# Optimization experiments

Measured on AMD Instinct MI355X. Metric: run time of the kernel, lower is better.

Reference implementation:

```python
import jax, jax.numpy as jnp
from jax import lax
import numpy as np

DIM = 192
HEADS = 8
TOPK = 2


def conv1x1(x, w):
    # x: [B,C,H,W], w: [O,C] (1x1 conv, no bias)
    return jnp.einsum('bchw,oc->bohw', x, w)


def setup_inputs() -> dict:
    key = jax.random.key(0)
    ks = jax.random.split(key, 6)
    B, C, H, W = 8, DIM, 128, 128
    x = jax.random.normal(ks[0], (B, C, H, W), jnp.float32)
    qkv_w = jax.random.normal(ks[1], (3 * C, C), jnp.float32) * 0.05
    dw_w = jax.random.normal(ks[2], (3 * C, 1, 3, 3), jnp.float32) * 0.1  # depthwise OIHW
    proj_w = jax.random.normal(ks[3], (C, C), jnp.float32) * 0.05
    router_main_w = jax.random.normal(ks[4], (HEADS, C), jnp.float32) * 0.05
    router_aux_w = jax.random.normal(ks[5], (HEADS, C), jnp.float32) * 0.05
    return dict(x=x, qkv_w=qkv_w, dw_w=dw_w, proj_w=proj_w,
                router_main_w=router_main_w, router_aux_w=router_aux_w,
                task_id=0)


def _forward(x, qkv_w, dw_w, proj_w, router_main_w, router_aux_w, task_id):
    B, C, H, W = x.shape
    heads, topk = HEADS, TOPK
    hd = C // heads
    N = H * W
    scale = hd ** -0.5

    # ---- router: softmax -> top-k -> mask -> renormalized gates ----
    rw = router_main_w if task_id == 0 else router_aux_w
    logits = jnp.einsum('bchw,oc->bohw', x, rw)                 # [B, heads, H, W]
    probs = jax.nn.softmax(
        logits.reshape(B, heads, N).transpose(0, 2, 1).reshape(B * N, heads), axis=1)
    _, idx = lax.top_k(probs, topk)                             # [B*N, topk]
    mask = lax.stop_gradient(
        jax.nn.one_hot(idx, heads, dtype=probs.dtype).sum(axis=1))  # [B*N, heads]
    masked = probs * mask
    denom = jnp.maximum(masked.sum(axis=1, keepdims=True), jnp.finfo(x.dtype).eps)
    gates = (masked / denom).reshape(B, N, heads).transpose(0, 2, 1)[:, :, None, :]  # [B, heads, 1, N]

    # ---- QKV: 1x1 conv + depthwise 3x3 conv ----
    qkv = conv1x1(x, qkv_w)                                      # [B, 3C, H, W]
    qkv = lax.conv_general_dilated(
        qkv, dw_w, window_strides=(1, 1), padding=((1, 1), (1, 1)),
        feature_group_count=3 * C,
        dimension_numbers=('NCHW', 'OIHW', 'NCHW'))
    q, k, v = jnp.split(qkv, 3, axis=1)

    def heads_view(t):  # b (h c) H W -> b h c (H W)
        return t.reshape(B, heads, hd, N)

    q, k, v = heads_view(q), heads_view(k), heads_view(v)
    # L2 normalize along the pixel axis (F.normalize, eps=1e-12)
    q = q / jnp.maximum(jnp.linalg.norm(q, axis=-1, keepdims=True), 1e-12)
    k = k / jnp.maximum(jnp.linalg.norm(k, axis=-1, keepdims=True), 1e-12)

    # channel attention: [B, heads, hd, hd] (tiny GEMM)
    attn = jax.nn.softmax(jnp.einsum('bhcn,bhdn->bhcd', q, k) * scale, axis=-1)
    out = jnp.einsum('bhcd,bhdn->bhcn', attn, v)                 # [B, heads, hd, N]

    out = out * gates * topk                                     # MoH gating
    out = out.reshape(B, C, H, W)                                # b (head c) h w
    out = conv1x1(out, proj_w)
    return out


def reference(x, qkv_w, dw_w, proj_w, router_main_w, router_aux_w, task_id):
    return _forward(x, qkv_w, dw_w, proj_w, router_main_w, router_aux_w, task_id)
```

## Files before the change

### kernel.cpp

```cpp
#include <hip/hip_runtime.h>
#include <hip/hip_bf16.h>

typedef __bf16 bf16;
typedef __bf16 bf16x8 __attribute__((ext_vector_type(8)));
typedef __bf16 bf16x4 __attribute__((ext_vector_type(4)));
typedef float f32x4 __attribute__((ext_vector_type(4)));
typedef unsigned int u32;

#define NPIX 16384
#define CDIM 192

__device__ __forceinline__ void gl2lds16(const bf16* g, const bf16* l) {
  __builtin_amdgcn_global_load_lds(
      (const __attribute__((address_space(1))) u32*)(g),
      (__attribute__((address_space(3))) u32*)(l), 16, 0, 0);
}

__global__ __launch_bounds__(256) void detect_kernel(
    const u32* __restrict__ xw, int* __restrict__ flag) {
  int tid = threadIdx.x;
  int cnt = 0;
  for (int i = 0; i < 32; i++) {
    u32 w = xw[tid * 32 + i];
    u32 e = (w >> 7) & 0xFFu;
    if (e >= 0xC0u) cnt++;
  }
  for (int off = 32; off; off >>= 1) cnt += __shfl_down(cnt, off);
  __shared__ int red[4];
  if ((tid & 63) == 0) red[tid >> 6] = cnt;
  __syncthreads();
  if (tid == 0) *flag = (red[0] + red[1] + red[2] + red[3] >= 16) ? 1 : 0;
}

__global__ __launch_bounds__(256) void wconvert_kernel(
    const void* __restrict__ s0, bf16* __restrict__ d0,
    const void* __restrict__ s1, bf16* __restrict__ d1,
    const void* __restrict__ s2, bf16* __restrict__ d2,
    const int* __restrict__ flag) {
  int which = blockIdx.y;
  const void* src = which == 0 ? s0 : (which == 1 ? s1 : s2);
  bf16* dst = which == 0 ? d0 : (which == 1 ? d1 : d2);
  int n = which == 0 ? 110592 : (which == 1 ? 5184 : 36864);
  int base = (blockIdx.x * 256 + threadIdx.x) * 8;
  if (base >= n) return;
  if (*flag) {
    const float* s = (const float*)src;
    float4 lo = *(const float4*)(s + base);
    float4 hi = *(const float4*)(s + base + 4);
    bf16x8 o;
    o[0] = (bf16)lo.x; o[1] = (bf16)lo.y; o[2] = (bf16)lo.z; o[3] = (bf16)lo.w;
    o[4] = (bf16)hi.x; o[5] = (bf16)hi.y; o[6] = (bf16)hi.z; o[7] = (bf16)hi.w;
    *(bf16x8*)(dst + base) = o;
  } else {
    *(bf16x8*)(dst + base) = *(const bf16x8*)((const bf16*)src + base);
  }
}

__global__ __launch_bounds__(256) void transpose_kernel(
    const void* __restrict__ xraw, bf16* __restrict__ xt,
    const int* __restrict__ flag) {
  int t = threadIdx.x;
  int b = blockIdx.y;
  int n0 = blockIdx.x * 128;
  int nl = (t & 31) * 4;
  int cb = (t >> 5) * 8;
  int f = *flag;
  for (int ch = 0; ch < 3; ch++) {
    int c8 = ch * 64 + cb;
    float v[8][4];
    if (f) {
      const float* xp = (const float*)xraw + ((size_t)b * CDIM << 14) + n0 + nl;
#pragma unroll
      for (int i = 0; i < 8; i++) {
        float4 q = *(const float4*)(xp + ((size_t)(c8 + i) << 14));
        v[i][0] = q.x; v[i][1] = q.y; v[i][2] = q.z; v[i][3] = q.w;
      }
    } else {
      const bf16* xp = (const bf16*)xraw + ((size_t)b * CDIM << 14) + n0 + nl;
#pragma unroll
      for (int i = 0; i < 8; i++) {
        bf16x4 q = *(const bf16x4*)(xp + ((size_t)(c8 + i) << 14));
#pragma unroll
        for (int j = 0; j < 4; j++) v[i][j] = (float)q[j];
      }
    }
#pragma unroll
    for (int j = 0; j < 4; j++) {
      bf16x8 o;
#pragma unroll
      for (int i = 0; i < 8; i++) o[i] = (bf16)v[i][j];
      *(bf16x8*)(xt + ((size_t)b << 14) * CDIM + (size_t)(n0 + nl + j) * CDIM + c8) = o;
    }
  }
}

__global__ __launch_bounds__(256) void router_kernel(
    const void* __restrict__ xraw, const void* __restrict__ wmain,
    const void* __restrict__ waux, const int* __restrict__ task,
    const int* __restrict__ flag, float* __restrict__ gates2) {
  __shared__ float w[8][CDIM];
  int tid = threadIdx.x;
  int f = *flag;
  const void* rw = (*task == 0) ? wmain : waux;
  for (int i = tid; i < 8 * CDIM; i += 256)
    w[i / CDIM][i % CDIM] = f ? ((const float*)rw)[i] : (float)((const bf16*)rw)[i];
  __syncthreads();
  int p = blockIdx.x * 256 + tid;
  int b = p >> 14, n = p & (NPIX - 1);
  float l[8];
#pragma unroll
  for (int h = 0; h < 8; h++) l[h] = 0.f;
  if (f) {
    const float* xb = (const float*)xraw + (((size_t)b * CDIM) << 14) + n;
    for (int c = 0; c < CDIM; c++) {
      float xv = xb[(size_t)c << 14];
#pragma unroll
      for (int h = 0; h < 8; h++) l[h] += xv * w[h][c];
    }
  } else {
    const bf16* xb = (const bf16*)xraw + (((size_t)b * CDIM) << 14) + n;
    for (int c = 0; c < CDIM; c++) {
      float xv = (float)xb[(size_t)c << 14];
#pragma unroll
      for (int h = 0; h < 8; h++) l[h] += xv * w[h][c];
    }
  }
  int i1 = 0;
#pragma unroll
  for (int h = 1; h < 8; h++) if (l[h] > l[i1]) i1 = h;
  int i2 = (i1 == 0) ? 1 : 0;
#pragma unroll
  for (int h = 0; h < 8; h++) if (h != i1 && l[h] > l[i2]) i2 = h;
  float e = __expf(l[i2] - l[i1]);
  float g1 = 2.f / (1.f + e);
  float g2 = e * g1;
  float* gb = gates2 + (((size_t)b * 8) << 14) + n;
#pragma unroll
  for (int h = 0; h < 8; h++) {
    float g = (h == i1) ? g1 : ((h == i2) ? g2 : 0.f);
    gb[(size_t)h << 14] = g;
  }
}

__global__ __launch_bounds__(256) void wgemm2_kernel(
    const bf16* __restrict__ A, const bf16* __restrict__ Xt,
    void* __restrict__ C, int M, const int* __restrict__ flag, int finalout) {
  __shared__ bf16 smem[22528];
  int tid = threadIdx.x;
  int wave = tid >> 6, lane = tid & 63;
  int c0 = lane & 15, qd = lane >> 4;

  int nm = M / 96;
  int ord = blockIdx.x + nm * (blockIdx.y + (blockIdx.z << 6));
  int z = ord & 7;
  int local = ord >> 3;
  int mt = local % nm;
  int nt = local / nm;
  int m0 = mt * 96, n0 = nt << 8;

  const bf16* Xb = Xt + (size_t)z * CDIM * NPIX;
  size_t cbase = (size_t)z * M * NPIX;

  int q = lane >> 4;
  int rr = (lane & 15) ^ (q << 1);
  const bf16* Ag0 = A + (size_t)(m0 + (wave << 4) + rr) * CDIM + (q << 3);
  const bf16* Ag1 = A + (size_t)(m0 + ((4 + wave) << 4) + rr) * CDIM + (q << 3);
  const bf16* Bg  = Xb + (size_t)(n0 + (wave << 6) + rr) * CDIM + (q << 3);

  int slot8 = ((qd << 4) + (c0 ^ (qd << 1))) << 3;

  f32x4 acc[6][4];
#pragma unroll
  for (int i = 0; i < 6; i++)
#pragma unroll
    for (int j = 0; j < 4; j++) acc[i][j] = {0.f, 0.f, 0.f, 0.f};

  auto STAGE = [&](int bb, int k) {
    gl2lds16(Ag0 + k, smem + bb + (wave << 9));
    if (wave < 2) gl2lds16(Ag1 + k, smem + bb + ((4 + wave) << 9));
    const bf16* bl = smem + bb + 3072 + (wave << 11);
    gl2lds16(Bg + k,             bl);
    gl2lds16(Bg + 16 * CDIM + k, bl + 512);
    gl2lds16(Bg + 32 * CDIM + k, bl + 1024);
    gl2lds16(Bg + 48 * CDIM + k, bl + 1536);
  };

  int bb = 0;
  STAGE(0, 0);
  __syncthreads();
  for (int t = 0; t < 6; t++) {
    if (t < 5) STAGE(bb ^ 11264, (t + 1) << 5);
    bf16x8 af[6], bfr[4];
#pragma unroll
    for (int mi = 0; mi < 6; mi++)
      af[mi] = *(const bf16x8*)(smem + bb + mi * 512 + slot8);
#pragma unroll
    for (int nj = 0; nj < 4; nj++)
      bfr[nj] = *(const bf16x8*)(smem + bb + 3072 + (wave << 11) + nj * 512 + slot8);
#pragma unroll
    for (int mi = 0; mi < 6; mi++)
#pragma unroll
      for (int nj = 0; nj < 4; nj++)
        acc[mi][nj] = __builtin_amdgcn_mfma_f32_16x16x32_bf16(af[mi], bfr[nj], acc[mi][nj], 0, 0, 0);
    if (t < 5) { __syncthreads(); bb ^= 11264; }
  }

  int f32o = finalout && (*flag);
#pragma unroll
  for (int mi = 0; mi < 6; mi++)
#pragma unroll
    for (int nj = 0; nj < 4; nj++)
#pragma unroll
      for (int r = 0; r < 4; r++) {
        int row = m0 + (mi << 4) + (qd << 2) + r;
        int col = n0 + (wave << 6) + (nj << 4) + c0;
        size_t idx = cbase + ((size_t)row << 14) + col;
        if (f32o) ((float*)C)[idx] = acc[mi][nj][r];
        else      ((bf16*)C)[idx]  = (bf16)acc[mi][nj][r];
      }
}

__global__ __launch_bounds__(256) void dwconv_kernel(
    const bf16* __restrict__ qkv, const bf16* __restrict__ w9,
    bf16* __restrict__ out, float* __restrict__ sumsq) {
  int tid = threadIdx.x;
  int ch = blockIdx.y, b = blockIdx.z;
  int xs = (tid & 15) << 3;
  int y0 = (blockIdx.x << 6) + ((tid >> 4) << 2);
  const bf16* in = qkv + (((size_t)(b * 576 + ch)) << 14);
  float wv[9];
#pragma unroll
  for (int i = 0; i < 9; i++) wv[i] = (float)w9[ch * 9 + i];
  float o[4][8];
#pragma unroll
  for (int r = 0; r < 4; r++)
#pragma unroll
    for (int i = 0; i < 8; i++) o[r][i] = 0.f;
#pragma unroll
  for (int rr = 0; rr < 6; rr++) {
    int yy = y0 - 1 + rr;
    if (yy < 0 || yy > 127) continue;
    const bf16* row = in + (yy << 7);
    float vals[10];
    vals[0] = (xs > 0) ? (float)row[xs - 1] : 0.f;
    bf16x8 v8 = *(const bf16x8*)(row + xs);
#pragma unroll
    for (int j = 0; j < 8; j++) vals[1 + j] = (float)v8[j];
    vals[9] = (xs < 120) ? (float)row[xs + 8] : 0.f;
#pragma unroll
    for (int orow = 0; orow < 4; orow++) {
      int wrow = rr - orow;
      if (wrow < 0 || wrow > 2) continue;
      float w0 = wv[wrow * 3 + 0], w1 = wv[wrow * 3 + 1], w2 = wv[wrow * 3 + 2];
#pragma unroll
      for (int i = 0; i < 8; i++)
        o[orow][i] += w0 * vals[i] + w1 * vals[i + 1] + w2 * vals[i + 2];
    }
  }
  float ss = 0.f;
  bf16* ob = out + (((size_t)(b * 576 + ch)) << 14);
#pragma unroll
  for (int r = 0; r < 4; r++) {
    bf16x8 ov;
#pragma unroll
    for (int i = 0; i < 8; i++) { ov[i] = (bf16)o[r][i]; ss += o[r][i] * o[r][i]; }
    *(bf16x8*)(ob + ((y0 + r) << 7) + xs) = ov;
  }
  if (ch < 384) {
#pragma unroll
    for (int off = 32; off; off >>= 1) ss += __shfl_down(ss, off);
    __shared__ float red[4];
    if ((tid & 63) == 0) red[tid >> 6] = ss;
    __syncthreads();
    if (tid == 0) atomicAdd(&sumsq[b * 384 + ch], red[0] + red[1] + red[2] + red[3]);
  }
}

__global__ __launch_bounds__(256) void spart_kernel(
    const bf16* __restrict__ dwout, float* __restrict__ Spart) {
  int tid = threadIdx.x;
  int bh = blockIdx.y, split = blockIdx.x;
  int b = bh >> 3, h = bh & 7;
  int wave = tid >> 6, lane = tid & 63;
  int c0 = lane & 15, qd = lane >> 4;
  __shared__ float Sred[576];
  for (int i = tid; i < 576; i += 256) Sred[i] = 0.f;
  __syncthreads();
  const bf16* qb = dwout + (((size_t)(b * 576 + h * 24)) << 14);
  const bf16* kb = dwout + (((size_t)(b * 576 + 192 + h * 24)) << 14);
  int r0 = c0;
  int r1 = (16 + c0 < 24) ? (16 + c0) : 23;
  f32x4 a00 = {0.f,0.f,0.f,0.f}, a01 = {0.f,0.f,0.f,0.f};
  f32x4 a10 = {0.f,0.f,0.f,0.f}, a11 = {0.f,0.f,0.f,0.f};
  int base = (((split << 2) + wave) << 9) + (qd << 3);
  for (int t = 0; t < 16; t++) {
    int kk = base + (t << 5);
    bf16x8 qa0 = *(const bf16x8*)(qb + (((size_t)r0) << 14) + kk);
    bf16x8 qa1 = *(const bf16x8*)(qb + (((size_t)r1) << 14) + kk);
    bf16x8 ka0 = *(const bf16x8*)(kb + (((size_t)r0) << 14) + kk);
    bf16x8 ka1 = *(const bf16x8*)(kb + (((size_t)r1) << 14) + kk);
    a00 = __builtin_amdgcn_mfma_f32_16x16x32_bf16(qa0, ka0, a00, 0, 0, 0);
    a01 = __builtin_amdgcn_mfma_f32_16x16x32_bf16(qa0, ka1, a01, 0, 0, 0);
    a10 = __builtin_amdgcn_mfma_f32_16x16x32_bf16(qa1, ka0, a10, 0, 0, 0);
    a11 = __builtin_amdgcn_mfma_f32_16x16x32_bf16(qa1, ka1, a11, 0, 0, 0);
  }
  f32x4 accs[4] = {a00, a01, a10, a11};
#pragma unroll
  for (int mi = 0; mi < 2; mi++)
#pragma unroll
    for (int nj = 0; nj < 2; nj++) {
      f32x4 a = accs[mi * 2 + nj];
#pragma unroll
      for (int r = 0; r < 4; r++) {
        int rrow = (mi << 4) + (qd << 2) + r;
        int cc = (nj << 4) + c0;
        if (rrow < 24 && cc < 24) atomicAdd(&Sred[rrow * 24 + cc], a[r]);
      }
    }
  __syncthreads();
  float* outp = Spart + (size_t)(bh * 8 + split) * 576;
  for (int i = tid; i < 576; i += 256) outp[i] = Sred[i];
}

__global__ __launch_bounds__(576) void attn_kernel(
    const float* __restrict__ Spart, const float* __restrict__ sumsq,
    float* __restrict__ attn) {
  int bh = blockIdx.x, tid = threadIdx.x;
  int b = bh >> 3, h = bh & 7;
  int c = tid / 24, d = tid % 24;
  float s = 0.f;
  for (int sp = 0; sp < 8; sp++) s += Spart[(size_t)(bh * 8 + sp) * 576 + tid];
  float nq = fmaxf(sqrtf(sumsq[b * 384 + h * 24 + c]), 1e-12f);
  float nk = fmaxf(sqrtf(sumsq[b * 384 + 192 + h * 24 + d]), 1e-12f);
  s = s / (nq * nk) * 0.20412414523193154f;
  __shared__ float Sm[576];
  Sm[tid] = s;
  __syncthreads();
  float mx = -1e30f;
  for (int j = 0; j < 24; j++) mx = fmaxf(mx, Sm[c * 24 + j]);
  float Z = 0.f;
  for (int j = 0; j < 24; j++) Z += __expf(Sm[c * 24 + j] - mx);
  attn[(size_t)bh * 576 + tid] = __expf(s - mx) / Z;
}

__global__ __launch_bounds__(256) void av_kernel(
    const bf16* __restrict__ dwout, const float* __restrict__ attn,
    const float* __restrict__ gates2, bf16* __restrict__ gated_t) {
  int tid = threadIdx.x;
  int bh = blockIdx.y;
  int b = bh >> 3, h = bh & 7;
  int n = blockIdx.x * 256 + tid;
  __shared__ float At[576];
  for (int i = tid; i < 576; i += 256) At[i] = attn[(size_t)bh * 576 + i];
  __syncthreads();
  const bf16* vb = dwout + (((size_t)(b * 576 + 384 + h * 24)) << 14) + n;
  float acc[24];
#pragma unroll
  for (int c = 0; c < 24; c++) acc[c] = 0.f;
#pragma unroll
  for (int d0 = 0; d0 < 24; d0 += 4) {
    float v0 = (float)vb[(size_t)(d0 + 0) << 14];
    float v1 = (float)vb[(size_t)(d0 + 1) << 14];
    float v2 = (float)vb[(size_t)(d0 + 2) << 14];
    float v3 = (float)vb[(size_t)(d0 + 3) << 14];
#pragma unroll
    for (int c = 0; c < 24; c++) {
      const float4* ap = (const float4*)&At[c * 24 + d0];
      acc[c] += ap->x * v0 + ap->y * v1 + ap->z * v2 + ap->w * v3;
    }
  }
  float g = gates2[(((size_t)(b * 8 + h)) << 14) + n];
  bf16* ob = gated_t + ((size_t)(b * NPIX + n)) * CDIM + h * 24;
#pragma unroll
  for (int ch = 0; ch < 3; ch++) {
    bf16x8 o;
#pragma unroll
    for (int i = 0; i < 8; i++) o[i] = (bf16)(acc[ch * 8 + i] * g);
    *(bf16x8*)(ob + ch * 8) = o;
  }
}

extern "C" void kernel_launch(void* const* d_in, const int* in_sizes, int n_in,
                              void* d_out, int out_size, void* d_ws, size_t ws_size,
                              hipStream_t stream) {
  const void* x_raw    = d_in[0];
  const void* qkvw_raw = d_in[1];
  const void* dww_raw  = d_in[2];
  const void* projw_raw= d_in[3];
  const void* rtm_raw  = d_in[4];
  const void* rta_raw  = d_in[5];
  const int*  task     = (const int*)d_in[6];
  char* ws = (char*)d_ws;

  bf16*  qkv_raw = (bf16*)(ws);
  bf16*  gated_t = qkv_raw;
  bf16*  dwout   = (bf16*)(ws + 150994944);
  float* gates2  = (float*)(ws + 301989888);
  float* sumsq   = (float*)(ws + 306184192);
  float* Spart   = (float*)(ws + 306196480);
  float* attn    = (float*)(ws + 307376128);
  int*   flag    = (int*)(ws + 307523584);
  bf16*  xt      = (bf16*)(ws + 307523712);
  bf16*  qkv_wb  = (bf16*)(ws + 357855360);
  bf16*  dw_wb   = (bf16*)(ws + 358076544);
  bf16*  proj_wb = (bf16*)(ws + 358086912);

  hipMemsetAsync(sumsq, 0, 8 * 384 * sizeof(float), stream);
  detect_kernel<<<1, 256, 0, stream>>>((const u32*)x_raw, flag);
  wconvert_kernel<<<dim3(54, 3), 256, 0, stream>>>(qkvw_raw, qkv_wb, dww_raw, dw_wb,
                                                   projw_raw, proj_wb, flag);
  transpose_kernel<<<dim3(128, 8), 256, 0, stream>>>(x_raw, xt, flag);
  router_kernel<<<512, 256, 0, stream>>>(x_raw, rtm_raw, rta_raw, task, flag, gates2);
  wgemm2_kernel<<<dim3(6, 64, 8), 256, 0, stream>>>(qkv_wb, xt, qkv_raw, 576, flag, 0);
  dwconv_kernel<<<dim3(2, 576, 8), 256, 0, stream>>>(qkv_raw, dw_wb, dwout, sumsq);
  spart_kernel<<<dim3(8, 64), 256, 0, stream>>>(dwout, Spart);
  attn_kernel<<<64, 576, 0, stream>>>(Spart, sumsq, attn);
  av_kernel<<<dim3(64, 64), 256, 0, stream>>>(dwout, attn, gates2, gated_t);
  wgemm2_kernel<<<dim3(2, 64, 8), 256, 0, stream>>>(proj_wb, gated_t, d_out, 192, flag, 1);
}
```

Before: 466.0 us.

## Fuse router logits into transpose kernel and vectorize GEMM epilogue stores

The router computation moves into the transpose kernel, reusing the x values already loaded there. Per-pixel logits are reduced across lanes with a shuffle and across waves through LDS before top-2 gating. This removes a separate full read of x, which is about 100MB in fp32. In the GEMM, the MFMA operands are swapped so each lane holds four consecutive columns, which lets the epilogue use vectorized float4/bf16x4 stores instead of scalar ones. The cost is extra LDS use and registers in the transpose kernel.

Result: faster. 448.5 us (-3.8%).

```diff
diff --git a/kernel.cpp b/kernel.cpp
--- a/kernel.cpp
+++ b/kernel.cpp
@@ -58,13 +58,28 @@
 
 __global__ __launch_bounds__(256) void transpose_kernel(
     const void* __restrict__ xraw, bf16* __restrict__ xt,
-    const int* __restrict__ flag) {
+    const int* __restrict__ flag, const void* __restrict__ wmain,
+    const void* __restrict__ waux, const int* __restrict__ task,
+    float* __restrict__ gates2) {
+  __shared__ float wT[CDIM][8];
+  __shared__ float lred[4][128][8];
   int t = threadIdx.x;
   int b = blockIdx.y;
   int n0 = blockIdx.x * 128;
+  int f = *flag;
+  const void* rw = (*task == 0) ? wmain : waux;
+  for (int i = t; i < 8 * CDIM; i += 256) {
+    int h = i / CDIM, c = i - h * CDIM;
+    wT[c][h] = f ? ((const float*)rw)[i] : (float)((const bf16*)rw)[i];
+  }
+  __syncthreads();
   int nl = (t & 31) * 4;
   int cb = (t >> 5) * 8;
-  int f = *flag;
+  float l[4][8];
+#pragma unroll
+  for (int j = 0; j < 4; j++)
+#pragma unroll
+    for (int h = 0; h < 8; h++) l[j][h] = 0.f;
   for (int ch = 0; ch < 3; ch++) {
     int c8 = ch * 64 + cb;
     float v[8][4];
@@ -85,6 +100,19 @@
       }
     }
 #pragma unroll
+    for (int i = 0; i < 8; i++) {
+      float4 wlo = *(const float4*)&wT[c8 + i][0];
+      float4 whi = *(const float4*)&wT[c8 + i][4];
+#pragma unroll
+      for (int j = 0; j < 4; j++) {
+        float xv = v[i][j];
+        l[j][0] += xv * wlo.x; l[j][1] += xv * wlo.y;
+        l[j][2] += xv * wlo.z; l[j][3] += xv * wlo.w;
+        l[j][4] += xv * whi.x; l[j][5] += xv * whi.y;
+        l[j][6] += xv * whi.z; l[j][7] += xv * whi.w;
+      }
+    }
+#pragma unroll
     for (int j = 0; j < 4; j++) {
       bf16x8 o;
 #pragma unroll
@@ -92,53 +120,37 @@
       *(bf16x8*)(xt + ((size_t)b << 14) * CDIM + (size_t)(n0 + nl + j) * CDIM + c8) = o;
     }
   }
-}
-
-__global__ __launch_bounds__(256) void router_kernel(
-    const void* __restrict__ xraw, const void* __restrict__ wmain,
-    const void* __restrict__ waux, const int* __restrict__ task,
-    const int* __restrict__ flag, float* __restrict__ gates2) {
-  __shared__ float w[8][CDIM];
-  int tid = threadIdx.x;
-  int f = *flag;
-  const void* rw = (*task == 0) ? wmain : waux;
-  for (int i = tid; i < 8 * CDIM; i += 256)
-    w[i / CDIM][i % CDIM] = f ? ((const float*)rw)[i] : (float)((const bf16*)rw)[i];
-  __syncthreads();
-  int p = blockIdx.x * 256 + tid;
-  int b = p >> 14, n = p & (NPIX - 1);
-  float l[8];
-#pragma unroll
-  for (int h = 0; h < 8; h++) l[h] = 0.f;
-  if (f) {
-    const float* xb = (const float*)xraw + (((size_t)b * CDIM) << 14) + n;
-    for (int c = 0; c < CDIM; c++) {
-      float xv = xb[(size_t)c << 14];
-#pragma unroll
-      for (int h = 0; h < 8; h++) l[h] += xv * w[h][c];
-    }
-  } else {
-    const bf16* xb = (const bf16*)xraw + (((size_t)b * CDIM) << 14) + n;
-    for (int c = 0; c < CDIM; c++) {
-      float xv = (float)xb[(size_t)c << 14];
-#pragma unroll
-      for (int h = 0; h < 8; h++) l[h] += xv * w[h][c];
-    }
-  }
-  int i1 = 0;
-#pragma unroll
-  for (int h = 1; h < 8; h++) if (l[h] > l[i1]) i1 = h;
-  int i2 = (i1 == 0) ? 1 : 0;
-#pragma unroll
-  for (int h = 0; h < 8; h++) if (h != i1 && l[h] > l[i2]) i2 = h;
-  float e = __expf(l[i2] - l[i1]);
-  float g1 = 2.f / (1.f + e);
-  float g2 = e * g1;
-  float* gb = gates2 + (((size_t)b * 8) << 14) + n;
-#pragma unroll
-  for (int h = 0; h < 8; h++) {
-    float g = (h == i1) ? g1 : ((h == i2) ? g2 : 0.f);
-    gb[(size_t)h << 14] = g;
+#pragma unroll
+  for (int j = 0; j < 4; j++)
+#pragma unroll
+    for (int h = 0; h < 8; h++) l[j][h] += __shfl_xor(l[j][h], 32);
+  int lane = t & 63, wid = t >> 6;
+  if (lane < 32) {
+#pragma unroll
+    for (int j = 0; j < 4; j++) {
+      *(float4*)&lred[wid][nl + j][0] = make_float4(l[j][0], l[j][1], l[j][2], l[j][3]);
+      *(float4*)&lred[wid][nl + j][4] = make_float4(l[j][4], l[j][5], l[j][6], l[j][7]);
+    }
+  }
+  __syncthreads();
+  if (t < 128) {
+    float lg[8];
+#pragma unroll
+    for (int h = 0; h < 8; h++)
+      lg[h] = (lred[0][t][h] + lred[1][t][h]) + (lred[2][t][h] + lred[3][t][h]);
+    int i1 = 0;
+#pragma unroll
+    for (int h = 1; h < 8; h++) if (lg[h] > lg[i1]) i1 = h;
+    int i2 = (i1 == 0) ? 1 : 0;
+#pragma unroll
+    for (int h = 0; h < 8; h++) if (h != i1 && lg[h] > lg[i2]) i2 = h;
+    float e = __expf(lg[i2] - lg[i1]);
+    float g1 = 2.f / (1.f + e);
+    float g2 = e * g1;
+    float* gb = gates2 + (((size_t)b * 8) << 14) + n0 + t;
+#pragma unroll
+    for (int h = 0; h < 8; h++)
+      gb[(size_t)h << 14] = (h == i1) ? g1 : ((h == i2) ? g2 : 0.f);
   }
 }
 
@@ -201,23 +213,28 @@
     for (int mi = 0; mi < 6; mi++)
 #pragma unroll
       for (int nj = 0; nj < 4; nj++)
-        acc[mi][nj] = __builtin_amdgcn_mfma_f32_16x16x32_bf16(af[mi], bfr[nj], acc[mi][nj], 0, 0, 0);
+        acc[mi][nj] = __builtin_amdgcn_mfma_f32_16x16x32_bf16(bfr[nj], af[mi], acc[mi][nj], 0, 0, 0);
     if (t < 5) { __syncthreads(); bb ^= 11264; }
   }
 
   int f32o = finalout && (*flag);
-#pragma unroll
-  for (int mi = 0; mi < 6; mi++)
-#pragma unroll
-    for (int nj = 0; nj < 4; nj++)
-#pragma unroll
-      for (int r = 0; r < 4; r++) {
-        int row = m0 + (mi << 4) + (qd << 2) + r;
-        int col = n0 + (wave << 6) + (nj << 4) + c0;
-        size_t idx = cbase + ((size_t)row << 14) + col;
-        if (f32o) ((float*)C)[idx] = acc[mi][nj][r];
-        else      ((bf16*)C)[idx]  = (bf16)acc[mi][nj][r];
+  int n_base = n0 + (wave << 6) + (qd << 2);
+#pragma unroll
+  for (int mi = 0; mi < 6; mi++) {
+    size_t rowb = cbase + ((size_t)(m0 + (mi << 4) + c0) << 14) + n_base;
+#pragma unroll
+    for (int nj = 0; nj < 4; nj++) {
+      if (f32o) {
+        *(float4*)((float*)C + rowb + (nj << 4)) =
+            make_float4(acc[mi][nj][0], acc[mi][nj][1], acc[mi][nj][2], acc[mi][nj][3]);
+      } else {
+        bf16x4 o;
+        o[0] = (bf16)acc[mi][nj][0]; o[1] = (bf16)acc[mi][nj][1];
+        o[2] = (bf16)acc[mi][nj][2]; o[3] = (bf16)acc[mi][nj][3];
+        *(bf16x4*)((bf16*)C + rowb + (nj << 4)) = o;
       }
+    }
+  }
 }
 
 __global__ __launch_bounds__(256) void dwconv_kernel(
@@ -409,8 +426,8 @@
   detect_kernel<<<1, 256, 0, stream>>>((const u32*)x_raw, flag);
   wconvert_kernel<<<dim3(54, 3), 256, 0, stream>>>(qkvw_raw, qkv_wb, dww_raw, dw_wb,
                                                    projw_raw, proj_wb, flag);
-  transpose_kernel<<<dim3(128, 8), 256, 0, stream>>>(x_raw, xt, flag);
-  router_kernel<<<512, 256, 0, stream>>>(x_raw, rtm_raw, rta_raw, task, flag, gates2);
+  transpose_kernel<<<dim3(128, 8), 256, 0, stream>>>(x_raw, xt, flag,
+                                                     rtm_raw, rta_raw, task, gates2);
   wgemm2_kernel<<<dim3(6, 64, 8), 256, 0, stream>>>(qkv_wb, xt, qkv_raw, 576, flag, 0);
   dwconv_kernel<<<dim3(2, 576, 8), 256, 0, stream>>>(qkv_raw, dw_wb, dwout, sumsq);
   spart_kernel<<<dim3(8, 64), 256, 0, stream>>>(dwout, Spart);
```
